# Performance work log

Measured on AMD Instinct MI355X. Metric: run time of the kernel, lower is better.

## Reference

```python
import jax, jax.numpy as jnp
import numpy as np

N = 8192
K = 8192
BS = 128  # quantization block size (elements per codebook)
NE = 8    # codebook entries per block (3-bit indices)


def setup_inputs() -> dict:
    key = jax.random.key(0)
    k1, k2, k3 = jax.random.split(key, 3)
    num_blocks = N * K // BS  # 524288
    n_packed_bytes = num_blocks * BS * 3 // 8  # 25165824
    x = jax.random.normal(k1, (2048, K), dtype=jnp.float32)
    # random packed bytes (values 0..255) -> uniformly random 3-bit indices
    packed_indices = jax.random.randint(k2, (n_packed_bytes,), 0, 256, dtype=jnp.int32)
    codebook = jax.random.normal(k3, (num_blocks, NE), dtype=jnp.float32)
    return {"x": x, "packed_indices": packed_indices, "codebook": codebook}


def _dequantize(packed_indices, codebook):
    num_blocks = codebook.shape[0]
    packed = packed_indices.reshape(-1, 3).astype(jnp.int32)  # (n_groups, 3)
    bits24 = packed[:, 0] | (packed[:, 1] << 8) | (packed[:, 2] << 16)
    shifts = jnp.arange(8, dtype=jnp.int32) * 3
    idx = (bits24[:, None] >> shifts[None, :]) & 7          # (n_groups, 8)
    idx = idx.reshape(num_blocks, BS)                        # (num_blocks, BS)
    # per-block codebook gather: w[b, i] = codebook[b, idx[b, i]]
    w = jnp.take_along_axis(codebook, idx, axis=1)           # (num_blocks, BS)
    return w.reshape(N, K)


def reference(x, packed_indices, codebook):
    w = _dequantize(packed_indices, codebook)  # (N, K) fp32
    y = x @ w.T                                # (batch, N)
    return y
```

## Files before the change

kernel.cpp:

```cpp
#include <hip/hip_runtime.h>
#include <hip/hip_bf16.h>

#define Mdim 2048
#define Ndim 8192
#define Kdim 8192
#define NT (Kdim / 64)

typedef __bf16 bf16x8 __attribute__((ext_vector_type(8)));
typedef float f32x4 __attribute__((ext_vector_type(4)));
typedef unsigned short ushort8 __attribute__((ext_vector_type(8)));
typedef unsigned short ushort4v __attribute__((ext_vector_type(4)));

__device__ __forceinline__ unsigned short f2bf_rne(float f) {
    unsigned u = __float_as_uint(f);
    u += 0x7fffu + ((u >> 16) & 1u);
    return (unsigned short)(u >> 16);
}

__device__ __forceinline__ ushort8 decode8(unsigned bits, float4 c0, float4 c1) {
    ushort8 o;
#pragma unroll
    for (int i = 0; i < 8; ++i) {
        unsigned id = (bits >> (3 * i)) & 7u;
        float a0 = (id & 1) ? c0.y : c0.x;
        float a1 = (id & 1) ? c0.w : c0.z;
        float a2 = (id & 1) ? c1.y : c1.x;
        float a3 = (id & 1) ? c1.w : c1.z;
        float b0 = (id & 2) ? a1 : a0;
        float b1 = (id & 2) ? a3 : a2;
        float v  = (id & 4) ? b1 : b0;
        o[i] = f2bf_rne(v);
    }
    return o;
}

__global__ __launch_bounds__(256) void k_prep(const int* __restrict__ packed,
                                              const float* __restrict__ cb,
                                              const float* __restrict__ x,
                                              unsigned short* __restrict__ W,
                                              unsigned short* __restrict__ xb) {
    const int t = threadIdx.x;
    if (blockIdx.x < 8192) {
        const size_t th = (size_t)blockIdx.x * 256 + t;
        const size_t g0 = th * 4;
        const int4* pv = (const int4*)(packed + g0 * 3);
        int4 q0 = pv[0], q1 = pv[1], q2 = pv[2];
        unsigned bits0 = (unsigned)(q0.x & 255) | ((unsigned)(q0.y & 255) << 8) |
                         ((unsigned)(q0.z & 255) << 16);
        unsigned bits1 = (unsigned)(q0.w & 255) | ((unsigned)(q1.x & 255) << 8) |
                         ((unsigned)(q1.y & 255) << 16);
        unsigned bits2 = (unsigned)(q1.z & 255) | ((unsigned)(q1.w & 255) << 8) |
                         ((unsigned)(q2.x & 255) << 16);
        unsigned bits3 = (unsigned)(q2.y & 255) | ((unsigned)(q2.z & 255) << 8) |
                         ((unsigned)(q2.w & 255) << 16);
        const float4* cv = (const float4*)(cb + ((g0 >> 4) << 3));
        float4 c0 = cv[0], c1 = cv[1];
        unsigned short* wp = W + (g0 << 3);
        *(ushort8*)(wp)      = decode8(bits0, c0, c1);
        *(ushort8*)(wp + 8)  = decode8(bits1, c0, c1);
        *(ushort8*)(wp + 16) = decode8(bits2, c0, c1);
        *(ushort8*)(wp + 24) = decode8(bits3, c0, c1);
    } else {
        const size_t u = (size_t)(blockIdx.x - 8192) * 256 + t;
        float4 a = ((const float4*)x)[u];
        ushort4v o;
        o[0] = f2bf_rne(a.x); o[1] = f2bf_rne(a.y);
        o[2] = f2bf_rne(a.z); o[3] = f2bf_rne(a.w);
        ((ushort4v*)xb)[u] = o;
    }
}

__device__ __forceinline__ void gld16(const unsigned short* g, unsigned short* l) {
    __builtin_amdgcn_global_load_lds(
        (const __attribute__((address_space(1))) unsigned int*)g,
        (__attribute__((address_space(3))) unsigned int*)l, 16, 0, 0);
}

#define BAR()    asm volatile("s_barrier" ::: "memory")
#define FENCE()  asm volatile("" ::: "memory")
#define SBAR0()  __builtin_amdgcn_sched_barrier(0)
#define VMCNT(n) asm volatile("s_waitcnt vmcnt(" #n ")" ::: "memory")

__global__ __launch_bounds__(512, 2) void k_gemm(const unsigned short* __restrict__ A,
                                                 const unsigned short* __restrict__ B,
                                                 float* __restrict__ C) {
    __shared__ unsigned short LA[4 * 8192];
    __shared__ unsigned short LB[4 * 8192];

    const int tid  = threadIdx.x;
    const int lane = tid & 63;
    const int wave = tid >> 6;
    const int qm = wave >> 2;
    const int qn = wave & 3;

    const int bid = blockIdx.x;
    const int bm = (bid & 7) * 256;
    const int bn = (bid >> 3) * 256;

    const int chunk0 = tid, chunk1 = tid + 512;
    const int srow0 = chunk0 >> 3, srow1 = chunk1 >> 3;
    const int scol0 = ((chunk0 & 7) ^ (srow0 & 7)) * 8;
    const int scol1 = ((chunk1 & 7) ^ (srow1 & 7)) * 8;
    const unsigned short* Ag0 = A + (size_t)(bm + srow0) * Kdim + scol0;
    const unsigned short* Ag1 = A + (size_t)(bm + srow1) * Kdim + scol1;
    const unsigned short* Bg0 = B + (size_t)(bn + srow0) * Kdim + scol0;
    const unsigned short* Bg1 = B + (size_t)(bn + srow1) * Kdim + scol1;

#define STAGE_A(T, H, BUF) do {                                                   \
    unsigned short* _d = LA + ((BUF) * 2 + (H)) * 8192;                           \
    gld16(Ag0 + (size_t)(H) * 128 * Kdim + (size_t)(T) * 64, _d + (size_t)tid * 8);        \
    gld16(Ag1 + (size_t)(H) * 128 * Kdim + (size_t)(T) * 64, _d + (size_t)(tid + 512) * 8);\
    FENCE();                                                                      \
} while (0)
#define STAGE_B(T, H, BUF) do {                                                   \
    unsigned short* _d = LB + ((BUF) * 2 + (H)) * 8192;                           \
    gld16(Bg0 + (size_t)(H) * 128 * Kdim + (size_t)(T) * 64, _d + (size_t)tid * 8);        \
    gld16(Bg1 + (size_t)(H) * 128 * Kdim + (size_t)(T) * 64, _d + (size_t)(tid + 512) * 8);\
    FENCE();                                                                      \
} while (0)

    const int r15 = lane & 15;
    const int q   = lane >> 4;
    const int rlo = r15 & 7;
    const int aro = qm * 64 + r15;
    const int bro = qn * 32 + r15;
    const int ch0 = ((0 + q) ^ rlo) * 8;
    const int ch1 = ((4 + q) ^ rlo) * 8;

    f32x4 acc[4][4][2];
    const f32x4 zero = {0.f, 0.f, 0.f, 0.f};
#pragma unroll
    for (int p = 0; p < 4; ++p)
#pragma unroll
        for (int i = 0; i < 4; ++i)
#pragma unroll
            for (int j = 0; j < 2; ++j) acc[p][i][j] = zero;

    bf16x8 aF[4][2];
    bf16x8 bX[2][2][2];
    bf16x8 bY[2][2][2];

#define LOAD_AF(BUF, H) do {                                                      \
    const unsigned short* _s = LA + ((BUF) * 2 + (H)) * 8192;                     \
    _Pragma("unroll") for (int i = 0; i < 4; ++i) {                               \
        int _r = (aro + i * 16) * 64;                                             \
        aF[i][0] = *(const bf16x8*)&_s[_r + ch0];                                 \
        aF[i][1] = *(const bf16x8*)&_s[_r + ch1];                                 \
    }                                                                             \
} while (0)
#define LOAD_BALL(BUF, BSET) do {                                                 \
    _Pragma("unroll") for (int _h = 0; _h < 2; ++_h) {                            \
        const unsigned short* _s = LB + ((BUF) * 2 + _h) * 8192;                  \
        _Pragma("unroll") for (int j = 0; j < 2; ++j) {                           \
            int _r = (bro + j * 16) * 64;                                         \
            BSET[_h][j][0] = *(const bf16x8*)&_s[_r + ch0];                       \
            BSET[_h][j][1] = *(const bf16x8*)&_s[_r + ch1];                       \
        }                                                                         \
    }                                                                             \
} while (0)

#define MFMA_PH(P, BSET, H) do {                                                  \
    __builtin_amdgcn_s_setprio(1);                                                \
    _Pragma("unroll") for (int i = 0; i < 4; ++i)                                 \
    _Pragma("unroll") for (int j = 0; j < 2; ++j) {                               \
        acc[P][i][j] = __builtin_amdgcn_mfma_f32_16x16x32_bf16(                   \
            aF[i][0], BSET[(H)][j][0], acc[P][i][j], 0, 0, 0);                    \
        acc[P][i][j] = __builtin_amdgcn_mfma_f32_16x16x32_bf16(                   \
            aF[i][1], BSET[(H)][j][1], acc[P][i][j], 0, 0, 0);                    \
    }                                                                             \
    __builtin_amdgcn_s_setprio(0);                                                \
} while (0)

#define KSTEP(T, BUF, BCUR, BNXT) do {                                            \
                                                                          \
    if ((T) + 1 < NT) { VMCNT(6); STAGE_A((T) + 1, 1, (BUF) ^ 1); }               \
    else              { VMCNT(0); }                                               \
    MFMA_PH(0, BCUR, 0);                                                          \
    BAR();                                                                        \
                                                                          \
    if ((T) + 1 < NT) { VMCNT(4); }                                               \
    if ((T) + 2 < NT) STAGE_B((T) + 2, 0, BUF);                                   \
    MFMA_PH(1, BCUR, 1);                                                          \
    SBAR0();                                                                      \
    LOAD_AF(BUF, 1);                      \
    BAR();                                                                        \
                                                                          \
    if ((T) + 1 < NT) {                                                           \
        if ((T) + 2 < NT) { VMCNT(4); } else { VMCNT(2); }                        \
        LOAD_BALL((BUF) ^ 1, BNXT);                                               \
    }                                                                             \
    if ((T) + 2 < NT) STAGE_B((T) + 2, 1, BUF);                                   \
    MFMA_PH(2, BCUR, 1);                                                          \
    BAR();                                                                        \
                                                                          \
    if ((T) + 2 < NT) STAGE_A((T) + 2, 0, BUF);                                   \
    MFMA_PH(3, BCUR, 0);                                                          \
    SBAR0();                                                                      \
    if ((T) + 1 < NT) LOAD_AF((BUF) ^ 1, 0);                \
    BAR();                                                                        \
} while (0)

    STAGE_B(0, 0, 0); STAGE_B(0, 1, 0); STAGE_A(0, 0, 0); STAGE_A(0, 1, 0);
    STAGE_B(1, 0, 1); STAGE_B(1, 1, 1); STAGE_A(1, 0, 1);
    asm volatile("s_waitcnt vmcnt(8)" ::: "memory");
    BAR();
    LOAD_BALL(0, bX);
    LOAD_AF(0, 0);

    for (int t2 = 0; t2 < NT; t2 += 2) {
        KSTEP(t2, 0, bX, bY);
        KSTEP(t2 + 1, 1, bY, bX);
    }

    constexpr int RHs[4] = {0, 0, 1, 1};
    constexpr int CHs[4] = {0, 1, 1, 0};
#pragma unroll
    for (int p = 0; p < 4; ++p) {
#pragma unroll
        for (int i = 0; i < 4; ++i) {
#pragma unroll
            for (int j = 0; j < 2; ++j) {
                int row = bm + RHs[p] * 128 + qm * 64 + i * 16 + q * 4;
                int col = bn + CHs[p] * 128 + qn * 32 + j * 16 + r15;
                float* outp = C + (size_t)row * Ndim + col;
#pragma unroll
                for (int r = 0; r < 4; ++r)
                    outp[(size_t)r * Ndim] = acc[p][i][j][r];
            }
        }
    }

#undef STAGE_A
#undef STAGE_B
#undef LOAD_AF
#undef LOAD_BALL
#undef MFMA_PH
#undef KSTEP
}

extern "C" void kernel_launch(void* const* d_in, const int* in_sizes, int n_in,
                              void* d_out, int out_size, void* d_ws, size_t ws_size,
                              hipStream_t stream) {
    const float* x      = (const float*)d_in[0];
    const int*   packed = (const int*)d_in[1];
    const float* cb     = (const float*)d_in[2];
    float* out = (float*)d_out;

    unsigned short* Wb = (unsigned short*)d_ws;
    unsigned short* Xb = (unsigned short*)d_ws + (size_t)Ndim * Kdim;

    k_prep<<<24576, 256, 0, stream>>>(packed, cb, x, Wb, Xb);
    k_gemm<<<dim3(256), 512, 0, stream>>>(Xb, Wb, out);
}
```

Measured before the change: 471.3 us.

## Fuse 3-bit codebook dequantization into GEMM B-tile staging

```diff
diff --git a/kernel.cpp b/kernel.cpp
--- a/kernel.cpp
+++ b/kernel.cpp
@@ -8,7 +8,6 @@
 
 typedef __bf16 bf16x8 __attribute__((ext_vector_type(8)));
 typedef float f32x4 __attribute__((ext_vector_type(4)));
-typedef unsigned short ushort8 __attribute__((ext_vector_type(8)));
 typedef unsigned short ushort4v __attribute__((ext_vector_type(4)));
 
 __device__ __forceinline__ unsigned short f2bf_rne(float f) {
@@ -17,57 +16,14 @@
     return (unsigned short)(u >> 16);
 }
 
-__device__ __forceinline__ ushort8 decode8(unsigned bits, float4 c0, float4 c1) {
-    ushort8 o;
-#pragma unroll
-    for (int i = 0; i < 8; ++i) {
-        unsigned id = (bits >> (3 * i)) & 7u;
-        float a0 = (id & 1) ? c0.y : c0.x;
-        float a1 = (id & 1) ? c0.w : c0.z;
-        float a2 = (id & 1) ? c1.y : c1.x;
-        float a3 = (id & 1) ? c1.w : c1.z;
-        float b0 = (id & 2) ? a1 : a0;
-        float b1 = (id & 2) ? a3 : a2;
-        float v  = (id & 4) ? b1 : b0;
-        o[i] = f2bf_rne(v);
-    }
-    return o;
-}
-
-__global__ __launch_bounds__(256) void k_prep(const int* __restrict__ packed,
-                                              const float* __restrict__ cb,
-                                              const float* __restrict__ x,
-                                              unsigned short* __restrict__ W,
+__global__ __launch_bounds__(256) void k_prep(const float* __restrict__ x,
                                               unsigned short* __restrict__ xb) {
-    const int t = threadIdx.x;
-    if (blockIdx.x < 8192) {
-        const size_t th = (size_t)blockIdx.x * 256 + t;
-        const size_t g0 = th * 4;
-        const int4* pv = (const int4*)(packed + g0 * 3);
-        int4 q0 = pv[0], q1 = pv[1], q2 = pv[2];
-        unsigned bits0 = (unsigned)(q0.x & 255) | ((unsigned)(q0.y & 255) << 8) |
-                         ((unsigned)(q0.z & 255) << 16);
-        unsigned bits1 = (unsigned)(q0.w & 255) | ((unsigned)(q1.x & 255) << 8) |
-                         ((unsigned)(q1.y & 255) << 16);
-        unsigned bits2 = (unsigned)(q1.z & 255) | ((unsigned)(q1.w & 255) << 8) |
-                         ((unsigned)(q2.x & 255) << 16);
-        unsigned bits3 = (unsigned)(q2.y & 255) | ((unsigned)(q2.z & 255) << 8) |
-                         ((unsigned)(q2.w & 255) << 16);
-        const float4* cv = (const float4*)(cb + ((g0 >> 4) << 3));
-        float4 c0 = cv[0], c1 = cv[1];
-        unsigned short* wp = W + (g0 << 3);
-        *(ushort8*)(wp)      = decode8(bits0, c0, c1);
-        *(ushort8*)(wp + 8)  = decode8(bits1, c0, c1);
-        *(ushort8*)(wp + 16) = decode8(bits2, c0, c1);
-        *(ushort8*)(wp + 24) = decode8(bits3, c0, c1);
-    } else {
-        const size_t u = (size_t)(blockIdx.x - 8192) * 256 + t;
-        float4 a = ((const float4*)x)[u];
-        ushort4v o;
-        o[0] = f2bf_rne(a.x); o[1] = f2bf_rne(a.y);
-        o[2] = f2bf_rne(a.z); o[3] = f2bf_rne(a.w);
-        ((ushort4v*)xb)[u] = o;
-    }
+    const size_t u = (size_t)blockIdx.x * 256 + threadIdx.x;
+    float4 a = ((const float4*)x)[u];
+    ushort4v o;
+    o[0] = f2bf_rne(a.x); o[1] = f2bf_rne(a.y);
+    o[2] = f2bf_rne(a.z); o[3] = f2bf_rne(a.w);
+    ((ushort4v*)xb)[u] = o;
 }
 
 __device__ __forceinline__ void gld16(const unsigned short* g, unsigned short* l) {
@@ -79,10 +35,30 @@
 #define BAR()    asm volatile("s_barrier" ::: "memory")
 #define FENCE()  asm volatile("" ::: "memory")
 #define SBAR0()  __builtin_amdgcn_sched_barrier(0)
+#define LGKM0()  asm volatile("s_waitcnt lgkmcnt(0)" ::: "memory")
 #define VMCNT(n) asm volatile("s_waitcnt vmcnt(" #n ")" ::: "memory")
 
+__device__ __forceinline__ uint4 dec_group(unsigned b, unsigned P0, unsigned P1,
+                                           unsigned P2, unsigned P3) {
+    uint4 o;
+#pragma unroll
+    for (int k = 0; k < 4; ++k) {
+        unsigned ia = (b >> (6 * k)) & 3u;
+        unsigned ib = (b >> (6 * k + 3)) & 3u;
+        unsigned sel = ia * 0x0202u + 0x01000100u + ((ib * 0x0202u) << 16);
+        unsigned lo = __builtin_amdgcn_perm(P1, P0, sel);
+        unsigned hi = __builtin_amdgcn_perm(P3, P2, sel);
+        unsigned mA = (unsigned)((int)(b << (29 - 6 * k)) >> 31);
+        unsigned mB = (unsigned)((int)(b << (26 - 6 * k)) >> 31);
+        unsigned m = (mA & 0xFFFFu) | (mB & 0xFFFF0000u);
+        (&o.x)[k] = (hi & m) | (lo & ~m);
+    }
+    return o;
+}
+
 __global__ __launch_bounds__(512, 2) void k_gemm(const unsigned short* __restrict__ A,
-                                                 const unsigned short* __restrict__ B,
+                                                 const int* __restrict__ packed,
+                                                 const float* __restrict__ cb,
                                                  float* __restrict__ C) {
     __shared__ unsigned short LA[4 * 8192];
     __shared__ unsigned short LB[4 * 8192];
@@ -103,8 +79,6 @@
     const int scol1 = ((chunk1 & 7) ^ (srow1 & 7)) * 8;
     const unsigned short* Ag0 = A + (size_t)(bm + srow0) * Kdim + scol0;
     const unsigned short* Ag1 = A + (size_t)(bm + srow1) * Kdim + scol1;
-    const unsigned short* Bg0 = B + (size_t)(bn + srow0) * Kdim + scol0;
-    const unsigned short* Bg1 = B + (size_t)(bn + srow1) * Kdim + scol1;
 
 #define STAGE_A(T, H, BUF) do {                                                   \
     unsigned short* _d = LA + ((BUF) * 2 + (H)) * 8192;                           \
@@ -112,11 +86,40 @@
     gld16(Ag1 + (size_t)(H) * 128 * Kdim + (size_t)(T) * 64, _d + (size_t)(tid + 512) * 8);\
     FENCE();                                                                      \
 } while (0)
-#define STAGE_B(T, H, BUF) do {                                                   \
-    unsigned short* _d = LB + ((BUF) * 2 + (H)) * 8192;                           \
-    gld16(Bg0 + (size_t)(H) * 128 * Kdim + (size_t)(T) * 64, _d + (size_t)tid * 8);        \
-    gld16(Bg1 + (size_t)(H) * 128 * Kdim + (size_t)(T) * 64, _d + (size_t)(tid + 512) * 8);\
-    FENCE();                                                                      \
+
+    const int drow  = tid >> 1;
+    const int dp    = tid & 1;
+    const int dhalf = drow >> 7;
+    const int drr   = drow & 127;
+    const int drlo  = drr & 7;
+    const int dp4   = dp * 4;
+    const int nrow  = bn + drow;
+    const int* Pg   = packed + (size_t)nrow * 3072 + dp * 12;
+    const float* Cg = cb + (size_t)nrow * 512;
+
+    int4 bq0, bq1, bq2;
+    float4 bc0, bc1;
+    unsigned cP0, cP1, cP2, cP3;
+
+#define B_ISSUE(T3) do {                                                          \
+    const int4* _pp = (const int4*)(Pg + (size_t)(T3) * 24);                      \
+    bq0 = _pp[0]; bq1 = _pp[1]; bq2 = _pp[2];                                     \
+    const float4* _cp = (const float4*)(Cg + ((T3) >> 1) * 8);                    \
+    bc0 = _cp[0]; bc1 = _cp[1];                                                   \
+} while (0)
+
+#define CVT_CP(CC0, CC1) do {                                                     \
+    cP0 = (unsigned)f2bf_rne(CC0.x) | ((unsigned)f2bf_rne(CC0.y) << 16);          \
+    cP1 = (unsigned)f2bf_rne(CC0.z) | ((unsigned)f2bf_rne(CC0.w) << 16);          \
+    cP2 = (unsigned)f2bf_rne(CC1.x) | ((unsigned)f2bf_rne(CC1.y) << 16);          \
+    cP3 = (unsigned)f2bf_rne(CC1.z) | ((unsigned)f2bf_rne(CC1.w) << 16);          \
+} while (0)
+
+#define DECODE_G(G, W0, W1, W2, BUF) do {                                         \
+    unsigned _b = (unsigned)(W0) | ((unsigned)(W1) << 8) | ((unsigned)(W2) << 16);\
+    uint4 _o = dec_group(_b, cP0, cP1, cP2, cP3);                                 \
+    int _c = (dp4 + (G)) ^ drlo;                                                  \
+    *(uint4*)&LB[((BUF) * 2 + dhalf) * 8192 + drr * 64 + (_c << 3)] = _o;         \
 } while (0)
 
     const int r15 = lane & 15;
@@ -137,8 +140,8 @@
             for (int j = 0; j < 2; ++j) acc[p][i][j] = zero;
 
     bf16x8 aF[4][2];
-    bf16x8 bX[2][2][2];
-    bf16x8 bY[2][2][2];
+    bf16x8 bLo[2][2];
+    bf16x8 bHi[2][2];
 
 #define LOAD_AF(BUF, H) do {                                                      \
     const unsigned short* _s = LA + ((BUF) * 2 + (H)) * 8192;                     \
@@ -148,68 +151,86 @@
         aF[i][1] = *(const bf16x8*)&_s[_r + ch1];                                 \
     }                                                                             \
 } while (0)
-#define LOAD_BALL(BUF, BSET) do {                                                 \
-    _Pragma("unroll") for (int _h = 0; _h < 2; ++_h) {                            \
-        const unsigned short* _s = LB + ((BUF) * 2 + _h) * 8192;                  \
-        _Pragma("unroll") for (int j = 0; j < 2; ++j) {                           \
-            int _r = (bro + j * 16) * 64;                                         \
-            BSET[_h][j][0] = *(const bf16x8*)&_s[_r + ch0];                       \
-            BSET[_h][j][1] = *(const bf16x8*)&_s[_r + ch1];                       \
-        }                                                                         \
-    }                                                                             \
-} while (0)
-
-#define MFMA_PH(P, BSET, H) do {                                                  \
+#define LOAD_BF(SET, BUF, H) do {                                                 \
+    const unsigned short* _s = LB + ((BUF) * 2 + (H)) * 8192;                     \
+    _Pragma("unroll") for (int j = 0; j < 2; ++j) {                               \
+        int _r = (bro + j * 16) * 64;                                             \
+        SET[j][0] = *(const bf16x8*)&_s[_r + ch0];                                \
+        SET[j][1] = *(const bf16x8*)&_s[_r + ch1];                                \
+    }                                                                             \
+} while (0)
+
+#define MFMA_PH(P, SET) do {                                                      \
     __builtin_amdgcn_s_setprio(1);                                                \
     _Pragma("unroll") for (int i = 0; i < 4; ++i)                                 \
     _Pragma("unroll") for (int j = 0; j < 2; ++j) {                               \
         acc[P][i][j] = __builtin_amdgcn_mfma_f32_16x16x32_bf16(                   \
-            aF[i][0], BSET[(H)][j][0], acc[P][i][j], 0, 0, 0);                    \
+            aF[i][0], SET[j][0], acc[P][i][j], 0, 0, 0);                          \
         acc[P][i][j] = __builtin_amdgcn_mfma_f32_16x16x32_bf16(                   \
-            aF[i][1], BSET[(H)][j][1], acc[P][i][j], 0, 0, 0);                    \
+            aF[i][1], SET[j][1], acc[P][i][j], 0, 0, 0);                          \
     }                                                                             \
     __builtin_amdgcn_s_setprio(0);                                                \
 } while (0)
 
-#define KSTEP(T, BUF, BCUR, BNXT) do {                                            \
-                                                                          \
-    if ((T) + 1 < NT) { VMCNT(6); STAGE_A((T) + 1, 1, (BUF) ^ 1); }               \
-    else              { VMCNT(0); }                                               \
-    MFMA_PH(0, BCUR, 0);                                                          \
-    BAR();                                                                        \
-                                                                          \
-    if ((T) + 1 < NT) { VMCNT(4); }                                               \
-    if ((T) + 2 < NT) STAGE_B((T) + 2, 0, BUF);                                   \
-    MFMA_PH(1, BCUR, 1);                                                          \
+#define KSTEP(T, BUF) do {                                                        \
+                                                                          \
+    if ((T) + 1 < NT) STAGE_A((T) + 1, 1, (BUF) ^ 1);                             \
+    if ((T) + 2 < NT)      { VMCNT(9); }                                          \
+    else if ((T) + 1 < NT) { VMCNT(4); }                                          \
+    else                   { VMCNT(0); }                                          \
+    MFMA_PH(0, bLo);                                                              \
     SBAR0();                                                                      \
-    LOAD_AF(BUF, 1);                      \
-    BAR();                                                                        \
-                                                                          \
-    if ((T) + 1 < NT) {                                                           \
-        if ((T) + 2 < NT) { VMCNT(4); } else { VMCNT(2); }                        \
-        LOAD_BALL((BUF) ^ 1, BNXT);                                               \
-    }                                                                             \
-    if ((T) + 2 < NT) STAGE_B((T) + 2, 1, BUF);                                   \
-    MFMA_PH(2, BCUR, 1);                                                          \
-    BAR();                                                                        \
-                                                                          \
+    LOAD_BF(bHi, BUF, 1);                                   \
+    LGKM0(); BAR();                                                               \
+                                                                          \
+    if ((T) + 1 < NT) VMCNT(2);                                                   \
+    MFMA_PH(1, bHi);                                                              \
+    if ((T) + 2 < NT) {                                                           \
+        CVT_CP(bc0, bc1);                                                         \
+        DECODE_G(0, bq0.x, bq0.y, bq0.z, BUF);                                    \
+        DECODE_G(1, bq0.w, bq1.x, bq1.y, BUF);                                    \
+    }                                                                             \
+    SBAR0();                                                                      \
+    LOAD_AF(BUF, 1);                                        \
+    LGKM0(); BAR();                                                               \
+                                                                          \
+    MFMA_PH(2, bHi);                                                              \
+    if ((T) + 2 < NT) {                                                           \
+        DECODE_G(2, bq1.z, bq1.w, bq2.x, BUF);                                    \
+        DECODE_G(3, bq2.y, bq2.z, bq2.w, BUF);                                    \
+    }                                                                             \
+    LGKM0(); BAR();                                                               \
+                                                                          \
+    MFMA_PH(3, bLo);                                                              \
     if ((T) + 2 < NT) STAGE_A((T) + 2, 0, BUF);                                   \
-    MFMA_PH(3, BCUR, 0);                                                          \
+    if ((T) + 3 < NT) B_ISSUE((T) + 3);                                           \
     SBAR0();                                                                      \
-    if ((T) + 1 < NT) LOAD_AF((BUF) ^ 1, 0);                \
-    BAR();                                                                        \
-} while (0)
-
-    STAGE_B(0, 0, 0); STAGE_B(0, 1, 0); STAGE_A(0, 0, 0); STAGE_A(0, 1, 0);
-    STAGE_B(1, 0, 1); STAGE_B(1, 1, 1); STAGE_A(1, 0, 1);
-    asm volatile("s_waitcnt vmcnt(8)" ::: "memory");
-    BAR();
-    LOAD_BALL(0, bX);
+    if ((T) + 1 < NT) { LOAD_AF((BUF) ^ 1, 0); LOAD_BF(bLo, (BUF) ^ 1, 0); }      \
+    LGKM0(); BAR();                                                               \
+} while (0)
+
+    STAGE_A(0, 0, 0); STAGE_A(0, 1, 0); STAGE_A(1, 0, 1);
+#pragma unroll
+    for (int tt = 0; tt < 2; ++tt) {
+        const int4* pp = (const int4*)(Pg + (size_t)tt * 24);
+        int4 w0 = pp[0], w1 = pp[1], w2 = pp[2];
+        const float4* cp = (const float4*)(Cg);
+        float4 c0 = cp[0], c1 = cp[1];
+        CVT_CP(c0, c1);
+        DECODE_G(0, w0.x, w0.y, w0.z, tt);
+        DECODE_G(1, w0.w, w1.x, w1.y, tt);
+        DECODE_G(2, w1.z, w1.w, w2.x, tt);
+        DECODE_G(3, w2.y, w2.z, w2.w, tt);
+    }
+    B_ISSUE(2);
+    VMCNT(5);
+    LGKM0(); BAR();
     LOAD_AF(0, 0);
+    LOAD_BF(bLo, 0, 0);
 
     for (int t2 = 0; t2 < NT; t2 += 2) {
-        KSTEP(t2, 0, bX, bY);
-        KSTEP(t2 + 1, 1, bY, bX);
+        KSTEP(t2, 0);
+        KSTEP(t2 + 1, 1);
     }
 
     constexpr int RHs[4] = {0, 0, 1, 1};
@@ -231,9 +252,11 @@
     }
 
 #undef STAGE_A
-#undef STAGE_B
+#undef B_ISSUE
+#undef CVT_CP
+#undef DECODE_G
 #undef LOAD_AF
-#undef LOAD_BALL
+#undef LOAD_BF
 #undef MFMA_PH
 #undef KSTEP
 }
@@ -246,9 +269,8 @@
     const float* cb     = (const float*)d_in[2];
     float* out = (float*)d_out;
 
-    unsigned short* Wb = (unsigned short*)d_ws;
-    unsigned short* Xb = (unsigned short*)d_ws + (size_t)Ndim * Kdim;
-
-    k_prep<<<24576, 256, 0, stream>>>(packed, cb, x, Wb, Xb);
-    k_gemm<<<dim3(256), 512, 0, stream>>>(Xb, Wb, out);
-}
+    unsigned short* Xb = (unsigned short*)d_ws;
+
+    k_prep<<<16384, 256, 0, stream>>>(x, Xb);
+    k_gemm<<<dim3(256), 512, 0, stream>>>(Xb, packed, cb, out);
+}
```

Measured after the change: 659.5 us. 39.9% more time.

## Decode 3-bit weights with byte-permute on pre-converted bf16 codebook pairs

Applied to the files above, without the earlier changes.

```diff
diff --git a/kernel.cpp b/kernel.cpp
--- a/kernel.cpp
+++ b/kernel.cpp
@@ -8,7 +8,6 @@
 
 typedef __bf16 bf16x8 __attribute__((ext_vector_type(8)));
 typedef float f32x4 __attribute__((ext_vector_type(4)));
-typedef unsigned short ushort8 __attribute__((ext_vector_type(8)));
 typedef unsigned short ushort4v __attribute__((ext_vector_type(4)));
 
 __device__ __forceinline__ unsigned short f2bf_rne(float f) {
@@ -17,56 +16,60 @@
     return (unsigned short)(u >> 16);
 }
 
-__device__ __forceinline__ ushort8 decode8(unsigned bits, float4 c0, float4 c1) {
-    ushort8 o;
-#pragma unroll
-    for (int i = 0; i < 8; ++i) {
-        unsigned id = (bits >> (3 * i)) & 7u;
-        float a0 = (id & 1) ? c0.y : c0.x;
-        float a1 = (id & 1) ? c0.w : c0.z;
-        float a2 = (id & 1) ? c1.y : c1.x;
-        float a3 = (id & 1) ? c1.w : c1.z;
-        float b0 = (id & 2) ? a1 : a0;
-        float b1 = (id & 2) ? a3 : a2;
-        float v  = (id & 4) ? b1 : b0;
-        o[i] = f2bf_rne(v);
+__device__ __forceinline__ uint4 dec_group(unsigned b, unsigned P0, unsigned P1,
+                                           unsigned P2, unsigned P3) {
+    uint4 o;
+#pragma unroll
+    for (int k = 0; k < 4; ++k) {
+        unsigned ia = (b >> (6 * k)) & 3u;
+        unsigned ib = (b >> (6 * k + 3)) & 3u;
+        unsigned sel = ia * 0x0202u + 0x01000100u + ((ib * 0x0202u) << 16);
+        unsigned lo = __builtin_amdgcn_perm(P1, P0, sel);
+        unsigned hi = __builtin_amdgcn_perm(P3, P2, sel);
+        unsigned mA = (unsigned)((int)(b << (29 - 6 * k)) >> 31);
+        unsigned mB = (unsigned)((int)(b << (26 - 6 * k)) >> 31);
+        unsigned m = (mA & 0xFFFFu) | (mB & 0xFFFF0000u);
+        (&o.x)[k] = (hi & m) | (lo & ~m);
     }
     return o;
 }
 
-__global__ __launch_bounds__(256) void k_prep(const int* __restrict__ packed,
-                                              const float* __restrict__ cb,
-                                              const float* __restrict__ x,
-                                              unsigned short* __restrict__ W,
-                                              unsigned short* __restrict__ xb) {
-    const int t = threadIdx.x;
-    if (blockIdx.x < 8192) {
-        const size_t th = (size_t)blockIdx.x * 256 + t;
-        const size_t g0 = th * 4;
-        const int4* pv = (const int4*)(packed + g0 * 3);
-        int4 q0 = pv[0], q1 = pv[1], q2 = pv[2];
-        unsigned bits0 = (unsigned)(q0.x & 255) | ((unsigned)(q0.y & 255) << 8) |
-                         ((unsigned)(q0.z & 255) << 16);
-        unsigned bits1 = (unsigned)(q0.w & 255) | ((unsigned)(q1.x & 255) << 8) |
-                         ((unsigned)(q1.y & 255) << 16);
-        unsigned bits2 = (unsigned)(q1.z & 255) | ((unsigned)(q1.w & 255) << 8) |
-                         ((unsigned)(q2.x & 255) << 16);
-        unsigned bits3 = (unsigned)(q2.y & 255) | ((unsigned)(q2.z & 255) << 8) |
-                         ((unsigned)(q2.w & 255) << 16);
-        const float4* cv = (const float4*)(cb + ((g0 >> 4) << 3));
-        float4 c0 = cv[0], c1 = cv[1];
-        unsigned short* wp = W + (g0 << 3);
-        *(ushort8*)(wp)      = decode8(bits0, c0, c1);
-        *(ushort8*)(wp + 8)  = decode8(bits1, c0, c1);
-        *(ushort8*)(wp + 16) = decode8(bits2, c0, c1);
-        *(ushort8*)(wp + 24) = decode8(bits3, c0, c1);
-    } else {
-        const size_t u = (size_t)(blockIdx.x - 8192) * 256 + t;
+__global__ __launch_bounds__(256) void k_prep_x(const float* __restrict__ x,
+                                                unsigned short* __restrict__ xb) {
+    for (size_t u = (size_t)blockIdx.x * 256 + threadIdx.x; u < 4194304u;
+         u += 524288u) {
         float4 a = ((const float4*)x)[u];
         ushort4v o;
         o[0] = f2bf_rne(a.x); o[1] = f2bf_rne(a.y);
         o[2] = f2bf_rne(a.z); o[3] = f2bf_rne(a.w);
         ((ushort4v*)xb)[u] = o;
+    }
+}
+
+__global__ __launch_bounds__(256) void k_prep_w(const int* __restrict__ packed,
+                                                const float* __restrict__ cb,
+                                                unsigned short* __restrict__ W) {
+#pragma unroll 2
+    for (size_t th = (size_t)blockIdx.x * 256 + threadIdx.x; th < 2097152u;
+         th += 524288u) {
+        const size_t g0 = th * 4;
+        const int4* pv = (const int4*)(packed + g0 * 3);
+        int4 q0 = pv[0], q1 = pv[1], q2 = pv[2];
+        const float4* cv = (const float4*)(cb + ((g0 >> 4) << 3));
+        float4 c0 = cv[0], c1 = cv[1];
+        unsigned cP0 = (unsigned)f2bf_rne(c0.x) | ((unsigned)f2bf_rne(c0.y) << 16);
+        unsigned cP1 = (unsigned)f2bf_rne(c0.z) | ((unsigned)f2bf_rne(c0.w) << 16);
+        unsigned cP2 = (unsigned)f2bf_rne(c1.x) | ((unsigned)f2bf_rne(c1.y) << 16);
+        unsigned cP3 = (unsigned)f2bf_rne(c1.z) | ((unsigned)f2bf_rne(c1.w) << 16);
+        unsigned bits0 = (unsigned)q0.x | ((unsigned)q0.y << 8) | ((unsigned)q0.z << 16);
+        unsigned bits1 = (unsigned)q0.w | ((unsigned)q1.x << 8) | ((unsigned)q1.y << 16);
+        unsigned bits2 = (unsigned)q1.z | ((unsigned)q1.w << 8) | ((unsigned)q2.x << 16);
+        unsigned bits3 = (unsigned)q2.y | ((unsigned)q2.z << 8) | ((unsigned)q2.w << 16);
+        unsigned short* wp = W + (g0 << 3);
+        *(uint4*)(wp)      = dec_group(bits0, cP0, cP1, cP2, cP3);
+        *(uint4*)(wp + 8)  = dec_group(bits1, cP0, cP1, cP2, cP3);
+        *(uint4*)(wp + 16) = dec_group(bits2, cP0, cP1, cP2, cP3);
+        *(uint4*)(wp + 24) = dec_group(bits3, cP0, cP1, cP2, cP3);
     }
 }
 
@@ -249,6 +252,7 @@
     unsigned short* Wb = (unsigned short*)d_ws;
     unsigned short* Xb = (unsigned short*)d_ws + (size_t)Ndim * Kdim;
 
-    k_prep<<<24576, 256, 0, stream>>>(packed, cb, x, Wb, Xb);
+    k_prep_x<<<2048, 256, 0, stream>>>(x, Xb);
+    k_prep_w<<<2048, 256, 0, stream>>>(packed, cb, Wb);
     k_gemm<<<dim3(256), 512, 0, stream>>>(Xb, Wb, out);
 }
```

After: 525.5 us. +11.5%, slower.

## Halve per-thread dequant work and reorder GEMM tile mapping to iterate N fastest

Applied to the files above, without the earlier changes.

```diff
diff --git a/kernel.cpp b/kernel.cpp
--- a/kernel.cpp
+++ b/kernel.cpp
@@ -40,28 +40,26 @@
                                               unsigned short* __restrict__ W,
                                               unsigned short* __restrict__ xb) {
     const int t = threadIdx.x;
-    if (blockIdx.x < 8192) {
+    if (blockIdx.x < 16384) {
         const size_t th = (size_t)blockIdx.x * 256 + t;
-        const size_t g0 = th * 4;
-        const int4* pv = (const int4*)(packed + g0 * 3);
-        int4 q0 = pv[0], q1 = pv[1], q2 = pv[2];
+        const size_t g0 = th * 2;
+        const int2* pv = (const int2*)(packed + g0 * 3);
+        int2 q0 = pv[0], q1 = pv[1], q2 = pv[2];
         unsigned bits0 = (unsigned)(q0.x & 255) | ((unsigned)(q0.y & 255) << 8) |
-                         ((unsigned)(q0.z & 255) << 16);
-        unsigned bits1 = (unsigned)(q0.w & 255) | ((unsigned)(q1.x & 255) << 8) |
-                         ((unsigned)(q1.y & 255) << 16);
-        unsigned bits2 = (unsigned)(q1.z & 255) | ((unsigned)(q1.w & 255) << 8) |
-                         ((unsigned)(q2.x & 255) << 16);
-        unsigned bits3 = (unsigned)(q2.y & 255) | ((unsigned)(q2.z & 255) << 8) |
-                         ((unsigned)(q2.w & 255) << 16);
-        const float4* cv = (const float4*)(cb + ((g0 >> 4) << 3));
-        float4 c0 = cv[0], c1 = cv[1];
+                         ((unsigned)(q1.x & 255) << 16);
+        unsigned bits1 = (unsigned)(q1.y & 255) | ((unsigned)(q2.x & 255) << 8) |
+                         ((unsigned)(q2.y & 255) << 16);
+        const float4* cv0 = (const float4*)(cb + ((g0 >> 4) << 3));
+        const float4* cv1 = (const float4*)(cb + (((g0 + 1) >> 4) << 3));
+        float4 c00 = cv0[0], c01 = cv0[1];
+        float4 c10 = cv1[0], c11 = cv1[1];
+        ushort8 o0 = decode8(bits0, c00, c01);
+        ushort8 o1 = decode8(bits1, c10, c11);
         unsigned short* wp = W + (g0 << 3);
-        *(ushort8*)(wp)      = decode8(bits0, c0, c1);
-        *(ushort8*)(wp + 8)  = decode8(bits1, c0, c1);
-        *(ushort8*)(wp + 16) = decode8(bits2, c0, c1);
-        *(ushort8*)(wp + 24) = decode8(bits3, c0, c1);
+        *(ushort8*)(wp)     = o0;
+        *(ushort8*)(wp + 8) = o1;
     } else {
-        const size_t u = (size_t)(blockIdx.x - 8192) * 256 + t;
+        const size_t u = (size_t)(blockIdx.x - 16384) * 256 + t;
         float4 a = ((const float4*)x)[u];
         ushort4v o;
         o[0] = f2bf_rne(a.x); o[1] = f2bf_rne(a.y);
@@ -94,8 +92,8 @@
     const int qn = wave & 3;
 
     const int bid = blockIdx.x;
-    const int bm = (bid & 7) * 256;
-    const int bn = (bid >> 3) * 256;
+    const int bm = (bid >> 5) * 256;
+    const int bn = (bid & 31) * 256;
 
     const int chunk0 = tid, chunk1 = tid + 512;
     const int srow0 = chunk0 >> 3, srow1 = chunk1 >> 3;
@@ -249,6 +247,6 @@
     unsigned short* Wb = (unsigned short*)d_ws;
     unsigned short* Xb = (unsigned short*)d_ws + (size_t)Ndim * Kdim;
 
-    k_prep<<<24576, 256, 0, stream>>>(packed, cb, x, Wb, Xb);
+    k_prep<<<32768, 256, 0, stream>>>(packed, cb, x, Wb, Xb);
     k_gemm<<<dim3(256), 512, 0, stream>>>(Xb, Wb, out);
 }
```

New measurement: 458.1 us. 2.8% less time.
